# Optimization experiments

Hardware: AMD Instinct MI355X
Metric: run time of the kernel (lower is better)

## Reference

```python
import jax, jax.numpy as jnp
import numpy as np

B, N, E = 4, 10000, 160000
F_EXOG = 8
IN_DIM = 9          # 1 (pm25) + F_EXOG
HIST, PRED = 8, 12
HID = 64
GNN_OUT = 13
E_HID, E_OUT = 32, 30
GRU_IN = IN_DIM + GNN_OUT  # 22


def setup_inputs() -> dict:
    key = jax.random.key(0)
    ks = jax.random.split(key, 16)
    s = 0.1
    return {
        "pm25_hist": jax.random.normal(ks[0], (B, HIST, N, 1), jnp.float32),
        "feature": jax.random.normal(ks[1], (B, HIST + PRED, N, F_EXOG), jnp.float32),
        "edge_attr": jax.random.uniform(ks[2], (E, 2), jnp.float32),
        "wind_mean": jnp.array([2.0, 180.0], jnp.float32),
        "wind_std": jnp.array([1.5, 90.0], jnp.float32),
        # edge MLP: Linear(21->32), Sigmoid, Linear(32->30), Sigmoid
        "e_w1": jax.random.normal(ks[3], (2 * IN_DIM + 3, E_HID), jnp.float32) * s,
        "e_b1": jnp.zeros((E_HID,), jnp.float32),
        "e_w2": jax.random.normal(ks[4], (E_HID, E_OUT), jnp.float32) * s,
        "e_b2": jnp.zeros((E_OUT,), jnp.float32),
        # node MLP: Linear(30->13), Sigmoid
        "n_w": jax.random.normal(ks[5], (E_OUT, GNN_OUT), jnp.float32) * s,
        "n_b": jnp.zeros((GNN_OUT,), jnp.float32),
        # GRUCell(22 -> 64), torch layout: weight_ih (3H, in), weight_hh (3H, H)
        "gru_wi": jax.random.normal(ks[6], (3 * HID, GRU_IN), jnp.float32) * s,
        "gru_wh": jax.random.normal(ks[7], (3 * HID, HID), jnp.float32) * s,
        "gru_bi": jnp.zeros((3 * HID,), jnp.float32),
        "gru_bh": jnp.zeros((3 * HID,), jnp.float32),
        # fc_out: Linear(64 -> 1)
        "fc_w": jax.random.normal(ks[8], (HID, 1), jnp.float32) * s,
        "fc_b": jnp.zeros((1,), jnp.float32),
        "edge_index": jax.random.randint(ks[9], (2, E), 0, N, jnp.int64),
    }


def _forward(pm25_hist, feature, edge_attr, wind_mean, wind_std,
             e_w1, e_b1, e_w2, e_b2, n_w, n_b,
             gru_wi, gru_wh, gru_bi, gru_bh, fc_w, fc_b, edge_index):
    batch, _, n_nodes, _ = pm25_hist.shape
    src, tgt = edge_index[0], edge_index[1]

    # buffers precomputed in __init__ (torch.std uses ddof=1)
    edge_mean = edge_attr.mean(axis=0, keepdims=True)
    edge_std = jnp.maximum(jnp.std(edge_attr, axis=0, ddof=1, keepdims=True), 1e-6)
    edge_attr_norm = (edge_attr - edge_mean) / edge_std          # (E, 2)
    city_dist = jnp.maximum(edge_attr[:, 0], 1e-3)               # (E,)
    city_direc = edge_attr[:, 1]                                 # (E,)
    w_std = jnp.maximum(wind_std, 1e-6)

    def graph_gnn(x):                                            # x: (B, N, IN_DIM)
        node_src = x[:, src]                                     # (B, E, IN_DIM)
        node_tgt = x[:, tgt]
        wind = node_src[..., -2:] * w_std + wind_mean            # de-normalize
        speed = jnp.maximum(wind[..., 0], 0.0)                   # (B, E)
        wdir = jnp.deg2rad(wind[..., 1])
        theta = jnp.abs(city_direc - wdir)
        edge_w = jax.nn.relu(3.0 * speed * jnp.cos(theta) / city_dist)  # (B, E)
        ean = jnp.broadcast_to(edge_attr_norm, (x.shape[0], E, 2))
        h = jnp.concatenate([node_src, node_tgt, ean, edge_w[..., None]], axis=-1)
        h = jax.nn.sigmoid(h @ e_w1 + e_b1)
        h = jax.nn.sigmoid(h @ e_w2 + e_b2)                      # (B, E, E_OUT)
        agg = jnp.zeros((x.shape[0], n_nodes, E_OUT), x.dtype)
        agg = agg.at[:, tgt].add(h).at[:, src].add(-h)           # scatter add / sub
        return jax.nn.sigmoid(agg @ n_w + n_b)                   # (B, N, GNN_OUT)

    def gru_step(h, x):                                          # h,x: (B*N, .)
        gi = x @ gru_wi.T + gru_bi
        gh = h @ gru_wh.T + gru_bh
        i_r, i_z, i_n = jnp.split(gi, 3, axis=-1)
        h_r, h_z, h_n = jnp.split(gh, 3, axis=-1)
        r = jax.nn.sigmoid(i_r + h_r)
        z = jax.nn.sigmoid(i_z + h_z)
        n = jnp.tanh(i_n + r * h_n)
        return (1.0 - z) * n + z * h

    def step(carry, feat_t):
        hn, xn = carry                                           # (B*N,HID), (B,N,1)
        x = jnp.concatenate([xn, feat_t], axis=-1)               # (B, N, IN_DIM)
        x_gnn = graph_gnn(x)
        xc = jnp.concatenate([x_gnn, x], axis=-1).reshape(batch * n_nodes, -1)
        hn = gru_step(hn, xc)
        xn = hn.reshape(batch, n_nodes, HID) @ fc_w + fc_b       # (B, N, 1)
        return (hn, xn), xn[..., 0]

    hn0 = jnp.zeros((batch * n_nodes, HID), pm25_hist.dtype)
    xn0 = pm25_hist[:, -1]                                       # (B, N, 1)
    feats = jnp.swapaxes(feature[:, HIST:HIST + PRED], 0, 1)     # (PRED, B, N, F)
    _, preds = jax.lax.scan(step, (hn0, xn0), feats)             # (PRED, B, N)
    return jnp.transpose(preds, (1, 2, 0))                       # (B, N, PRED)


def reference(pm25_hist, feature, edge_attr, wind_mean, wind_std,
              e_w1, e_b1, e_w2, e_b2, n_w, n_b,
              gru_wi, gru_wh, gru_bi, gru_bh, fc_w, fc_b, edge_index):
    return _forward(pm25_hist, feature, edge_attr, wind_mean, wind_std,
                    e_w1, e_b1, e_w2, e_b2, n_w, n_b,
                    gru_wi, gru_wh, gru_bi, gru_bh, fc_w, fc_b, edge_index)
```

## Files before the change

### kernel.cpp

```cpp
#include <hip/hip_runtime.h>
#include <hip/hip_fp16.h>
#include <cstddef>

#define BB    4
#define NN    10000
#define EE    160000
#define BN    40000
#define HISTC 8
#define PREDC 12
#define TSTEP 20
#define FEX   8
#define HIDC  64
#define EHID  32
#define EOUTC 30
#define GOUTC 13
#define GINC  22

typedef float v2f __attribute__((ext_vector_type(2)));
typedef _Float16 v2h __attribute__((ext_vector_type(2)));

struct alignas(16) WPack {
    __half2 w[16];
    float   nw[14];
    float   b2;
    float   pad;
};

__device__ __forceinline__ float fast_rcp(float x) { return __builtin_amdgcn_rcpf(x); }
__device__ __forceinline__ float sigm(float x) {
    return fast_rcp(1.0f + __expf(-x));
}
__device__ __forceinline__ v2f sigm2(v2f x) {
    v2f r; r.x = sigm(x.x); r.y = sigm(x.y); return r;
}
__device__ __forceinline__ float tanh_fast(float x) {
    x = fminf(fmaxf(x, -15.0f), 15.0f);
    float e = __expf(2.0f * x);
    return (e - 1.0f) * fast_rcp(e + 1.0f);
}

__device__ __forceinline__ float dot2(__half2 a, __half2 b, float c) {
#if __has_builtin(__builtin_amdgcn_fdot2)
    union { __half2 h; v2h v; } ua, ub;
    ua.h = a; ub.h = b;
    return __builtin_amdgcn_fdot2(ua.v, ub.v, c, false);
#else
    float2 fa = __half22float2(a), fb = __half22float2(b);
    return c + fa.x * fb.x + fa.y * fb.y;
#endif
}

__global__ __launch_bounds__(256) void stats1_kernel(const float* __restrict__ ea,
                                                     double* __restrict__ part) {
    __shared__ double sm[256][4];
    int tid = threadIdx.x;
    double s0 = 0, s1 = 0, q0 = 0, q1 = 0;
    for (int e = blockIdx.x * 256 + tid; e < EE; e += 256 * 256) {
        float2 v = reinterpret_cast<const float2*>(ea)[e];
        double v0 = (double)v.x, v1 = (double)v.y;
        s0 += v0; q0 += v0 * v0;
        s1 += v1; q1 += v1 * v1;
    }
    sm[tid][0] = s0; sm[tid][1] = s1; sm[tid][2] = q0; sm[tid][3] = q1;
    __syncthreads();
    for (int off = 128; off > 0; off >>= 1) {
        if (tid < off)
            for (int k = 0; k < 4; k++) sm[tid][k] += sm[tid + off][k];
        __syncthreads();
    }
    if (tid == 0) {
        part[blockIdx.x * 4 + 0] = sm[0][0];
        part[blockIdx.x * 4 + 1] = sm[0][1];
        part[blockIdx.x * 4 + 2] = sm[0][2];
        part[blockIdx.x * 4 + 3] = sm[0][3];
    }
}

__global__ __launch_bounds__(256) void stats2_kernel(const double* __restrict__ part,
                                                     float* __restrict__ stats) {
    __shared__ double sm[256][4];
    int tid = threadIdx.x;
    sm[tid][0] = part[tid * 4 + 0];
    sm[tid][1] = part[tid * 4 + 1];
    sm[tid][2] = part[tid * 4 + 2];
    sm[tid][3] = part[tid * 4 + 3];
    __syncthreads();
    for (int off = 128; off > 0; off >>= 1) {
        if (tid < off)
            for (int k = 0; k < 4; k++) sm[tid][k] += sm[tid + off][k];
        __syncthreads();
    }
    if (tid == 0) {
        double m0 = sm[0][0] / EE, m1 = sm[0][1] / EE;
        double v0 = (sm[0][2] - sm[0][0] * sm[0][0] / EE) / (double)(EE - 1);
        double v1 = (sm[0][3] - sm[0][1] * sm[0][1] / EE) / (double)(EE - 1);
        float sd0 = fmaxf((float)sqrt(v0 > 0 ? v0 : 0.0), 1e-6f);
        float sd1 = fmaxf((float)sqrt(v1 > 0 ? v1 : 0.0), 1e-6f);
        stats[0] = (float)m0; stats[1] = (float)m1;
        stats[2] = 1.0f / sd0; stats[3] = 1.0f / sd1;
    }
}

__global__ __launch_bounds__(256) void edgepre_kernel(
    const float* __restrict__ ea, const float* __restrict__ stats,
    const int* __restrict__ eidx,
    int* __restrict__ deg_t, int* __restrict__ deg_s,
    float4* __restrict__ epre4)
{
    int e = blockIdx.x * 256 + threadIdx.x;
    if (e >= EE) return;
    float2 v = reinterpret_cast<const float2*>(ea)[e];
    float4 r;
    r.x = (v.x - stats[0]) * stats[2];
    r.y = (v.y - stats[1]) * stats[3];
    r.z = 1.0f / fmaxf(v.x, 1e-3f);
    r.w = v.y;
    epre4[e] = r;
    atomicAdd(&deg_s[eidx[e]], 1);
    atomicAdd(&deg_t[eidx[EE + e]], 1);
}

__global__ __launch_bounds__(256) void cvtw_kernel(
    const float* __restrict__ wi, const float* __restrict__ wh,
    const float* __restrict__ ew2, const float* __restrict__ eb2,
    const float* __restrict__ nw,
    __half* __restrict__ wi_h, __half* __restrict__ wh_h,
    WPack* __restrict__ wpack)
{
    int i = blockIdx.x * 256 + threadIdx.x;
    if (i < 192 * GINC) wi_h[i] = __float2half(wi[i]);
    if (i < 192 * HIDC) wh_h[i] = __float2half(wh[i]);
    if (i < EOUTC) {
        WPack wp;
        #pragma unroll
        for (int q = 0; q < 16; q++)
            wp.w[q] = __floats2half2_rn(ew2[(2 * q) * EOUTC + i],
                                        ew2[(2 * q + 1) * EOUTC + i]);
        #pragma unroll
        for (int j = 0; j < GOUTC; j++) wp.nw[j] = nw[i * GOUTC + j];
        wp.nw[13] = 0.f;
        wp.b2 = eb2[i];
        wp.pad = 0.f;
        wpack[i] = wp;
    }
}

__global__ void initxn_kernel(const float* __restrict__ pm, float* __restrict__ xn) {
    int i = blockIdx.x * 256 + threadIdx.x;
    if (i >= BN) return;
    int b = i / NN, n = i - b * NN;
    xn[i] = pm[(b * HISTC + (HISTC - 1)) * NN + n];
}

__global__ __launch_bounds__(1024) void scan_kernel(
    const int* __restrict__ deg_t, const int* __restrict__ deg_s,
    int* __restrict__ off_t, int* __restrict__ off_s,
    int* __restrict__ cnt_t, int* __restrict__ cnt_s)
{
    __shared__ int pt[1024], ps[1024];
    int tid = threadIdx.x;
    int base = tid * 10;
    int st = 0, ss = 0;
    for (int k = 0; k < 10; k++) {
        int i = base + k;
        if (i < NN) { st += deg_t[i]; ss += deg_s[i]; }
    }
    pt[tid] = st; ps[tid] = ss;
    __syncthreads();
    for (int off = 1; off < 1024; off <<= 1) {
        int vt = (tid >= off) ? pt[tid - off] : 0;
        int vs = (tid >= off) ? ps[tid - off] : 0;
        __syncthreads();
        pt[tid] += vt; ps[tid] += vs;
        __syncthreads();
    }
    int ext = (tid == 0) ? 0 : pt[tid - 1];
    int exs = (tid == 0) ? 0 : ps[tid - 1];
    for (int k = 0; k < 10; k++) {
        int i = base + k;
        if (i < NN) {
            off_t[i] = ext; cnt_t[i] = ext;
            off_s[i] = exs; cnt_s[i] = exs;
            ext += deg_t[i]; exs += deg_s[i];
        }
    }
    if (tid == 0) { off_t[NN] = EE; off_s[NN] = EE; }
}

__global__ void fillperm_kernel(const int* __restrict__ eidx,
                                const float4* __restrict__ epre4,
                                int* __restrict__ cnt_t, int* __restrict__ cnt_s,
                                int4* __restrict__ eT, float4* __restrict__ epreT)
{
    int e = blockIdx.x * 256 + threadIdx.x;
    if (e >= EE) return;
    int s = eidx[e];
    int g = eidx[EE + e];
    int pt = atomicAdd(&cnt_t[g], 1);
    int ps = atomicAdd(&cnt_s[s], 1);
    int4 r; r.x = s; r.y = g; r.z = ps; r.w = 0;
    eT[pt] = r;
    epreT[pt] = epre4[e];
}

__global__ __launch_bounds__(256) void pre_kernel(
    float* __restrict__ xncur, const float* __restrict__ feature, int t,
    const float* __restrict__ xp,
    const float* __restrict__ fb,
    const float* __restrict__ ew1,
    const float* __restrict__ wmean, const float* __restrict__ wstd,
    __half* __restrict__ preS, __half* __restrict__ preT,
    float2* __restrict__ wind2, float* __restrict__ out)
{
    __shared__ alignas(16) float w1s[18 * EHID];
    for (int i = threadIdx.x; i < 18 * EHID; i += 256) w1s[i] = ew1[i];
    __syncthreads();
    int idx = blockIdx.x * 256 + threadIdx.x;
    if (idx >= BN * 8) return;
    int i = idx >> 3;
    int c = idx & 7;
    int b = i / NN, n = i - b * NN;
    float x0;
    if (t == 0) {
        x0 = xncur[i];
    } else {
        x0 = (xp[i] + xp[BN + i]) + (xp[2 * BN + i] + xp[3 * BN + i]) + fb[0];
        if (c == 0) {
            xncur[i] = x0;
            out[(size_t)i * PREDC + (t - 1)] = x0;
        }
    }
    float x[9];
    x[0] = x0;
    {
        const float4* fp = reinterpret_cast<const float4*>(
            feature + (((size_t)b * TSTEP + HISTC + t) * NN + n) * FEX);
        float4 u = fp[0], v = fp[1];
        x[1] = u.x; x[2] = u.y; x[3] = u.z; x[4] = u.w;
        x[5] = v.x; x[6] = v.y; x[7] = v.z; x[8] = v.w;
    }
    float4 aS = {0.f, 0.f, 0.f, 0.f}, aT = {0.f, 0.f, 0.f, 0.f};
    #pragma unroll
    for (int k = 0; k < 9; k++) {
        float4 wS = reinterpret_cast<const float4*>(&w1s[k * EHID])[c];
        float4 wT = reinterpret_cast<const float4*>(&w1s[(9 + k) * EHID])[c];
        aS.x += x[k] * wS.x; aS.y += x[k] * wS.y; aS.z += x[k] * wS.z; aS.w += x[k] * wS.w;
        aT.x += x[k] * wT.x; aT.y += x[k] * wT.y; aT.z += x[k] * wT.z; aT.w += x[k] * wT.w;
    }
    union { uint2 u; __half h[4]; } sv, tv;
    sv.h[0] = __float2half(aS.x); sv.h[1] = __float2half(aS.y);
    sv.h[2] = __float2half(aS.z); sv.h[3] = __float2half(aS.w);
    tv.h[0] = __float2half(aT.x); tv.h[1] = __float2half(aT.y);
    tv.h[2] = __float2half(aT.z); tv.h[3] = __float2half(aT.w);
    reinterpret_cast<uint2*>(preS + (size_t)i * EHID)[c] = sv.u;
    reinterpret_cast<uint2*>(preT + (size_t)i * EHID)[c] = tv.u;
    if (c == 1) {
        float sd0 = fmaxf(wstd[0], 1e-6f), sd1 = fmaxf(wstd[1], 1e-6f);
        float speed = fmaxf(x[7] * sd0 + wmean[0], 0.f);
        float wdir  = (x[8] * sd1 + wmean[1]) * 0.017453292519943295f;
        float2 wv; wv.x = 3.0f * speed; wv.y = wdir;
        wind2[i] = wv;
    }
}

__global__ __launch_bounds__(256) void finalout_kernel(
    const float* __restrict__ xp, const float* __restrict__ fb,
    float* __restrict__ out)
{
    int i = blockIdx.x * 256 + threadIdx.x;
    if (i >= BN) return;
    out[(size_t)i * PREDC + (PREDC - 1)] =
        (xp[i] + xp[BN + i]) + (xp[2 * BN + i] + xp[3 * BN + i]) + fb[0];
}

__global__ __launch_bounds__(256) void edge_kernel(
    const int4* __restrict__ eT, const float4* __restrict__ epreT,
    const __half* __restrict__ preS, const __half* __restrict__ preT,
    const float2* __restrict__ wind2,
    const float* __restrict__ ew1, const float* __restrict__ eb1,
    const WPack* __restrict__ wpack,
    __half* __restrict__ h3t, __half* __restrict__ h3s)
{
    int i = blockIdx.x * 256 + threadIdx.x;
    int b = blockIdx.y;
    int4 et = eT[i];
    int s = et.x, g = et.y, ps = et.z;
    float4 ep = epreT[i];

    size_t iS = (size_t)b * NN + s, iT = (size_t)b * NN + g;
    float2 wv2 = wind2[iS];
    float ew = fmaxf(wv2.x * __cosf(fabsf(ep.w - wv2.y)) * ep.z, 0.f);

    union alignas(16) { uint4 u[4]; __half2 h2[16]; } RS, RT;
    {
        const uint4* p;
        p = reinterpret_cast<const uint4*>(preS + iS * EHID);
        RS.u[0] = p[0]; RS.u[1] = p[1]; RS.u[2] = p[2]; RS.u[3] = p[3];
        p = reinterpret_cast<const uint4*>(preT + iT * EHID);
        RT.u[0] = p[0]; RT.u[1] = p[1]; RT.u[2] = p[2]; RT.u[3] = p[3];
    }

    const v2f* W18 = reinterpret_cast<const v2f*>(ew1 + 18 * EHID);
    const v2f* W19 = reinterpret_cast<const v2f*>(ew1 + 19 * EHID);
    const v2f* W20 = reinterpret_cast<const v2f*>(ew1 + 20 * EHID);
    const v2f* B1  = reinterpret_cast<const v2f*>(eb1);
    float ean0 = ep.x, ean1 = ep.y;
    __half2 h1h[16];
    #pragma unroll
    for (int q = 0; q < 16; q++) {
        v2f u = W18[q] * ean0 + W19[q] * ean1 + B1[q] + W20[q] * ew;
        float2 rs = __half22float2(RS.h2[q]);
        float2 rt = __half22float2(RT.h2[q]);
        u.x += rs.x + rt.x;
        u.y += rs.y + rt.y;
        v2f sg = sigm2(u);
        h1h[q] = __floats2half2_rn(sg.x, sg.y);
    }

    v2f h3p[7];
    #pragma unroll
    for (int j = 0; j < 7; j++) { h3p[j].x = 0.f; h3p[j].y = 0.f; }
    for (int o = 0; o < EOUTC; o++) {
        const WPack* W = wpack + o;
        float acc0 = W->b2, acc1 = 0.f;
        #pragma unroll
        for (int q = 0; q < 16; q += 2) {
            acc0 = dot2(h1h[q],     W->w[q],     acc0);
            acc1 = dot2(h1h[q + 1], W->w[q + 1], acc1);
        }
        float h2v = sigm(acc0 + acc1);
        const v2f* nr = reinterpret_cast<const v2f*>(W->nw);
        #pragma unroll
        for (int j = 0; j < 7; j++) h3p[j] += nr[j] * h2v;
    }

    union alignas(16) { uint4 u[2]; __half2 h2[8]; } r;
    #pragma unroll
    for (int j = 0; j < 7; j++) r.h2[j] = __floats2half2_rn(h3p[j].x, h3p[j].y);
    r.h2[7] = __floats2half2_rn(0.f, 0.f);
    {
        __half* oT = h3t + ((size_t)b * EE + i) * 16;
        reinterpret_cast<uint4*>(oT)[0] = r.u[0];
        reinterpret_cast<uint4*>(oT)[1] = r.u[1];
        __half* oS = h3s + ((size_t)b * EE + ps) * 16;
        reinterpret_cast<uint4*>(oS)[0] = r.u[0];
        reinterpret_cast<uint4*>(oS)[1] = r.u[1];
    }
}

__global__ __launch_bounds__(256) void gather_kernel(
    const __half* __restrict__ h3t, const __half* __restrict__ h3s,
    const int* __restrict__ off_t, const int* __restrict__ off_s,
    const float* __restrict__ nb, const float* __restrict__ xncur,
    __half* __restrict__ xcagg)
{
    int n = (blockIdx.x * 256 + threadIdx.x) >> 6;
    if (n >= NN) return;
    n = __builtin_amdgcn_readfirstlane(n);
    int lane = threadIdx.x & 63;
    int b   = lane >> 4;
    int e4  = (lane >> 2) & 3;
    int chq = lane & 3;

    const __half* ht = h3t + (size_t)b * ((size_t)EE * 16) + chq * 4;
    const __half* hs = h3s + (size_t)b * ((size_t)EE * 16) + chq * 4;

    float a0 = 0.f, a1 = 0.f, a2 = 0.f, a3 = 0.f;
    {
        int i0 = off_t[n], i1 = off_t[n + 1];
        for (int i = i0 + e4; i < i1; i += 4) {
            uint2 v = *reinterpret_cast<const uint2*>(ht + (size_t)i * 16);
            float2 f01 = __half22float2(*reinterpret_cast<__half2*>(&v.x));
            float2 f23 = __half22float2(*reinterpret_cast<__half2*>(&v.y));
            a0 += f01.x; a1 += f01.y; a2 += f23.x; a3 += f23.y;
        }
    }
    {
        int i0 = off_s[n], i1 = off_s[n + 1];
        for (int i = i0 + e4; i < i1; i += 4) {
            uint2 v = *reinterpret_cast<const uint2*>(hs + (size_t)i * 16);
            float2 f01 = __half22float2(*reinterpret_cast<__half2*>(&v.x));
            float2 f23 = __half22float2(*reinterpret_cast<__half2*>(&v.y));
            a0 -= f01.x; a1 -= f01.y; a2 -= f23.x; a3 -= f23.y;
        }
    }
    a0 += __shfl_xor(a0, 4); a1 += __shfl_xor(a1, 4);
    a2 += __shfl_xor(a2, 4); a3 += __shfl_xor(a3, 4);
    a0 += __shfl_xor(a0, 8); a1 += __shfl_xor(a1, 8);
    a2 += __shfl_xor(a2, 8); a3 += __shfl_xor(a3, 8);

    if (e4 == 0) {
        int c0 = chq * 4;
        float nb0 = nb[c0 < GOUTC ? c0 : GOUTC - 1];
        float nb1 = nb[c0 + 1 < GOUTC ? c0 + 1 : GOUTC - 1];
        float nb2 = nb[c0 + 2 < GOUTC ? c0 + 2 : GOUTC - 1];
        float nb3 = nb[c0 + 3 < GOUTC ? c0 + 3 : GOUTC - 1];
        float v0 = (c0 + 0 < GOUTC) ? sigm(a0 + nb0) : 0.f;
        float v1 = (c0 + 1 < GOUTC) ? sigm(a1 + nb1)
                 : ((c0 + 1 == GOUTC) ? xncur[(size_t)b * NN + n] : 0.f);
        float v2 = (c0 + 2 < GOUTC) ? sigm(a2 + nb2) : 0.f;
        float v3 = (c0 + 3 < GOUTC) ? sigm(a3 + nb3) : 0.f;
        union { uint2 u; __half h[4]; } o;
        o.h[0] = __float2half(v0); o.h[1] = __float2half(v1);
        o.h[2] = __float2half(v2); o.h[3] = __float2half(v3);
        *reinterpret_cast<uint2*>(xcagg + ((size_t)b * NN + n) * 16 + c0) = o.u;
    }
}

__global__ __launch_bounds__(256) void node_kernel(
    const __half* __restrict__ xcagg, const float* __restrict__ feature, int t,
    const __half* __restrict__ wi_h, const __half* __restrict__ wh_h,
    const float* __restrict__ bi, const float* __restrict__ bh,
    const float* __restrict__ fw,
    const __half2* __restrict__ hnold, __half2* __restrict__ hnnew,
    float* __restrict__ xp)
{
    __shared__ float xpart[4][64];
    int lane = threadIdx.x & 63;
    int wav  = threadIdx.x >> 6;
    int jb   = blockIdx.y;
    int node = blockIdx.x * 64 + lane;
    int b = node / NN;
    int n = node - b * NN;

    __half2 xch[11];
    {
        union alignas(16) { uint4 u[2]; __half2 h2[8]; } X;
        const uint4* xp16 = reinterpret_cast<const uint4*>(xcagg + (size_t)node * 16);
        X.u[0] = xp16[0]; X.u[1] = xp16[1];
        #pragma unroll
        for (int p = 0; p < 7; p++) xch[p] = X.h2[p];
    }
    {
        const float4* fp = reinterpret_cast<const float4*>(
            feature + (((size_t)b * TSTEP + HISTC + t) * NN + n) * FEX);
        float4 u = fp[0], v = fp[1];
        xch[7]  = __floats2half2_rn(u.x, u.y);
        xch[8]  = __floats2half2_rn(u.z, u.w);
        xch[9]  = __floats2half2_rn(v.x, v.y);
        xch[10] = __floats2half2_rn(v.z, v.w);
    }

    __half2 hh[32];
    #pragma unroll
    for (int p = 0; p < 32; p++) hh[p] = hnold[(size_t)p * BN + node];

    float xsum = 0.f;
    #pragma unroll
    for (int jj2 = 0; jj2 < 2; jj2++) {
        int j0 = __builtin_amdgcn_readfirstlane(jb * 16 + wav * 4 + jj2 * 2);
        union { __half2 h; __half v[2]; } holdw;
        holdw.h = hnold[(size_t)(j0 >> 1) * BN + node];
        float hnew2[2];
        #pragma unroll
        for (int d = 0; d < 2; d++) {
            int j = j0 + d;
            float ir = bi[j], iz = bi[64 + j], in_ = bi[128 + j];
            const __half2* wr0 = reinterpret_cast<const __half2*>(wi_h + (size_t)j * GINC);
            const __half2* wr1 = reinterpret_cast<const __half2*>(wi_h + (size_t)(64 + j) * GINC);
            const __half2* wr2 = reinterpret_cast<const __half2*>(wi_h + (size_t)(128 + j) * GINC);
            #pragma unroll
            for (int p = 0; p < 11; p++) {
                ir  = dot2(xch[p], wr0[p], ir);
                iz  = dot2(xch[p], wr1[p], iz);
                in_ = dot2(xch[p], wr2[p], in_);
            }
            float hr0 = bh[j], hz0 = bh[64 + j], hn0 = bh[128 + j];
            float hr1 = 0.f, hz1 = 0.f, hn1 = 0.f;
            const __half2* vr0 = reinterpret_cast<const __half2*>(wh_h + (size_t)j * HIDC);
            const __half2* vr1 = reinterpret_cast<const __half2*>(wh_h + (size_t)(64 + j) * HIDC);
            const __half2* vr2 = reinterpret_cast<const __half2*>(wh_h + (size_t)(128 + j) * HIDC);
            #pragma unroll
            for (int p = 0; p < 32; p += 2) {
                hr0 = dot2(hh[p],     vr0[p],     hr0);
                hz0 = dot2(hh[p],     vr1[p],     hz0);
                hn0 = dot2(hh[p],     vr2[p],     hn0);
                hr1 = dot2(hh[p + 1], vr0[p + 1], hr1);
                hz1 = dot2(hh[p + 1], vr1[p + 1], hz1);
                hn1 = dot2(hh[p + 1], vr2[p + 1], hn1);
            }
            float r  = sigm(ir + hr0 + hr1);
            float z  = sigm(iz + hz0 + hz1);
            float nn = tanh_fast(in_ + r * (hn0 + hn1));
            float hold = __half2float(holdw.v[d]);
            float hnew = (1.f - z) * nn + z * hold;
            hnew2[d] = hnew;
            xsum += hnew * fw[j];
        }
        hnnew[(size_t)(j0 >> 1) * BN + node] = __floats2half2_rn(hnew2[0], hnew2[1]);
    }
    xpart[wav][lane] = xsum;
    __syncthreads();
    if (wav == 0) {
        float tot = xpart[0][lane] + xpart[1][lane] + xpart[2][lane] + xpart[3][lane];
        xp[(size_t)jb * BN + node] = tot;
    }
}

extern "C" void kernel_launch(void* const* d_in, const int* in_sizes, int n_in,
                              void* d_out, int out_size, void* d_ws, size_t ws_size,
                              hipStream_t stream)
{
    const float* pm    = (const float*)d_in[0];
    const float* feat  = (const float*)d_in[1];
    const float* ea    = (const float*)d_in[2];
    const float* wmean = (const float*)d_in[3];
    const float* wstd  = (const float*)d_in[4];
    const float* ew1   = (const float*)d_in[5];
    const float* eb1   = (const float*)d_in[6];
    const float* ew2   = (const float*)d_in[7];
    const float* eb2   = (const float*)d_in[8];
    const float* nw    = (const float*)d_in[9];
    const float* nb    = (const float*)d_in[10];
    const float* wi    = (const float*)d_in[11];
    const float* wh    = (const float*)d_in[12];
    const float* bi    = (const float*)d_in[13];
    const float* bh    = (const float*)d_in[14];
    const float* fw    = (const float*)d_in[15];
    const float* fb    = (const float*)d_in[16];
    const int*   eidx  = (const int*)d_in[17];
    float* out = (float*)d_out;

    char* w = (char*)d_ws;
    double* partd = (double*)w;                    w += 256 * 4 * sizeof(double);
    float*  stats = (float*)w;                     w += 16 * sizeof(float);
    WPack*  wpack = (WPack*)w;                     w += EOUTC * sizeof(WPack);
    float4* epre4 = (float4*)w;                    w += (size_t)EE * sizeof(float4);
    float4* epreT = (float4*)w;                    w += (size_t)EE * sizeof(float4);
    float*  xncur = (float*)w;                     w += (size_t)BN * sizeof(float);
    float*  xp    = (float*)w;                     w += (size_t)4 * BN * sizeof(float);
    __half2* hnA  = (__half2*)w;                   w += (size_t)32 * BN * sizeof(__half2);
    __half2* hnB  = (__half2*)w;                   w += (size_t)32 * BN * sizeof(__half2);
    __half* xcagg = (__half*)w;                    w += (size_t)BN * 16 * sizeof(__half);
    __half* preS  = (__half*)w;                    w += (size_t)BN * EHID * sizeof(__half);
    __half* preT  = (__half*)w;                    w += (size_t)BN * EHID * sizeof(__half);
    float2* wind2 = (float2*)w;                    w += (size_t)BN * sizeof(float2);
    __half* h3t   = (__half*)w;                    w += (size_t)BB * EE * 16 * sizeof(__half);
    __half* h3s   = (__half*)w;                    w += (size_t)BB * EE * 16 * sizeof(__half);
    __half* wi_h  = (__half*)w;                    w += (size_t)192 * GINC * sizeof(__half);
    __half* wh_h  = (__half*)w;                    w += (size_t)192 * HIDC * sizeof(__half);
    int*    deg_t = (int*)w;                       w += NN * sizeof(int);
    int*    deg_s = (int*)w;                       w += NN * sizeof(int);
    int*    off_t = (int*)w;                       w += (NN + 1) * sizeof(int);
    int*    off_s = (int*)w;                       w += (NN + 1) * sizeof(int);
    int*    cnt_t = (int*)w;                       w += NN * sizeof(int);
    int*    cnt_s = (int*)w;                       w += NN * sizeof(int);
    int4*   eT    = (int4*)w;                      w += (size_t)EE * sizeof(int4);

    stats1_kernel<<<256, 256, 0, stream>>>(ea, partd);
    stats2_kernel<<<1, 256, 0, stream>>>(partd, stats);
    hipMemsetAsync(deg_t, 0, 2 * NN * sizeof(int), stream);
    edgepre_kernel<<<(EE + 255) / 256, 256, 0, stream>>>(
        ea, stats, eidx, deg_t, deg_s, epre4);
    cvtw_kernel<<<(192 * HIDC + 255) / 256, 256, 0, stream>>>(
        wi, wh, ew2, eb2, nw, wi_h, wh_h, wpack);
    initxn_kernel<<<(BN + 255) / 256, 256, 0, stream>>>(pm, xncur);
    hipMemsetAsync(hnA, 0, (size_t)32 * BN * sizeof(__half2), stream);
    scan_kernel<<<1, 1024, 0, stream>>>(deg_t, deg_s, off_t, off_s, cnt_t, cnt_s);
    fillperm_kernel<<<(EE + 255) / 256, 256, 0, stream>>>(
        eidx, epre4, cnt_t, cnt_s, eT, epreT);

    for (int t = 0; t < PREDC; t++) {
        const __half2* hnold = (t & 1) ? hnB : hnA;
        __half2*       hnnew = (t & 1) ? hnA : hnB;
        pre_kernel<<<(BN * 8 + 255) / 256, 256, 0, stream>>>(
            xncur, feat, t, xp, fb, ew1, wmean, wstd, preS, preT, wind2, out);
        edge_kernel<<<dim3(EE / 256, BB), 256, 0, stream>>>(
            eT, epreT, preS, preT, wind2, ew1, eb1, wpack, h3t, h3s);
        gather_kernel<<<(NN * 64 + 255) / 256, 256, 0, stream>>>(
            h3t, h3s, off_t, off_s, nb, xncur, xcagg);
        node_kernel<<<dim3(BN / 64, 4), 256, 0, stream>>>(
            xcagg, feat, t, wi_h, wh_h, bi, bh, fw, hnold, hnnew, xp);
    }
    finalout_kernel<<<(BN + 255) / 256, 256, 0, stream>>>(xp, fb, out);
}
```

Baseline: 1.045 ms.

## Compute edge MLP second layer and node projection with MFMA matrix instructions

```diff
diff --git a/kernel.cpp b/kernel.cpp
--- a/kernel.cpp
+++ b/kernel.cpp
@@ -18,6 +18,8 @@
 
 typedef float v2f __attribute__((ext_vector_type(2)));
 typedef _Float16 v2h __attribute__((ext_vector_type(2)));
+typedef _Float16 v8h __attribute__((ext_vector_type(8)));
+typedef float f32x4 __attribute__((ext_vector_type(4)));
 
 struct alignas(16) WPack {
     __half2 w[16];
@@ -125,23 +127,19 @@
     const float* __restrict__ ew2, const float* __restrict__ eb2,
     const float* __restrict__ nw,
     __half* __restrict__ wi_h, __half* __restrict__ wh_h,
-    WPack* __restrict__ wpack)
+    __half* __restrict__ w2b, __half* __restrict__ nwb)
 {
     int i = blockIdx.x * 256 + threadIdx.x;
     if (i < 192 * GINC) wi_h[i] = __float2half(wi[i]);
     if (i < 192 * HIDC) wh_h[i] = __float2half(wh[i]);
-    if (i < EOUTC) {
-        WPack wp;
-        #pragma unroll
-        for (int q = 0; q < 16; q++)
-            wp.w[q] = __floats2half2_rn(ew2[(2 * q) * EOUTC + i],
-                                        ew2[(2 * q + 1) * EOUTC + i]);
-        #pragma unroll
-        for (int j = 0; j < GOUTC; j++) wp.nw[j] = nw[i * GOUTC + j];
-        wp.nw[13] = 0.f;
-        wp.b2 = eb2[i];
-        wp.pad = 0.f;
-        wpack[i] = wp;
+    if (i < 32 * 32) {
+        int o = i >> 5, k = i & 31;
+        w2b[i] = (o < EOUTC) ? __float2half(ew2[k * EOUTC + o]) : __half(0.0f);
+    }
+    if (i < 16 * 32) {
+        int j = i >> 5, o = i & 31;
+        nwb[i] = (j < GOUTC && o < EOUTC) ? __float2half(nw[o * GOUTC + j])
+                                          : __half(0.0f);
     }
 }
 
@@ -273,23 +271,43 @@
         (xp[i] + xp[BN + i]) + (xp[2 * BN + i] + xp[3 * BN + i]) + fb[0];
 }
 
+#define H1STR 40
+#define S2STR 36
 __global__ __launch_bounds__(256) void edge_kernel(
     const int4* __restrict__ eT, const float4* __restrict__ epreT,
     const __half* __restrict__ preS, const __half* __restrict__ preT,
     const float2* __restrict__ wind2,
     const float* __restrict__ ew1, const float* __restrict__ eb1,
-    const WPack* __restrict__ wpack,
+    const __half* __restrict__ w2b, const __half* __restrict__ nwb,
+    const float* __restrict__ eb2,
     __half* __restrict__ h3t, __half* __restrict__ h3s)
 {
-    int i = blockIdx.x * 256 + threadIdx.x;
+    __shared__ alignas(16) __half h1s[256 * H1STR];
+    __shared__ alignas(16) __half s2s[4][16 * S2STR];
+    __shared__ alignas(16) __half h3x[256 * 16];
+
+    int tid  = threadIdx.x;
+    int lane = tid & 63, wv = tid >> 6;
+    int l15  = lane & 15, lk = lane >> 4;
+    int i = blockIdx.x * 256 + tid;
     int b = blockIdx.y;
     int4 et = eT[i];
     int s = et.x, g = et.y, ps = et.z;
     float4 ep = epreT[i];
 
     size_t iS = (size_t)b * NN + s, iT = (size_t)b * NN + g;
-    float2 wv2 = wind2[iS];
-    float ew = fmaxf(wv2.x * __cosf(fabsf(ep.w - wv2.y)) * ep.z, 0.f);
+    float2 wvd = wind2[iS];
+    float ew = fmaxf(wvd.x * __cosf(fabsf(ep.w - wvd.y)) * ep.z, 0.f);
+
+    v8h bw2a, bw2b, bnw;
+    {
+        union { uint4 u; v8h h; } t;
+        t.u = *reinterpret_cast<const uint4*>(w2b + l15 * 32 + lk * 8);        bw2a = t.h;
+        t.u = *reinterpret_cast<const uint4*>(w2b + (16 + l15) * 32 + lk * 8); bw2b = t.h;
+        t.u = *reinterpret_cast<const uint4*>(nwb + l15 * 32 + lk * 8);        bnw  = t.h;
+    }
+    float b2v0 = eb2[l15];
+    float b2v1 = eb2[(16 + l15) < EOUTC ? (16 + l15) : (EOUTC - 1)];
 
     union alignas(16) { uint4 u[4]; __half2 h2[16]; } RS, RT;
     {
@@ -305,7 +323,7 @@
     const v2f* W20 = reinterpret_cast<const v2f*>(ew1 + 20 * EHID);
     const v2f* B1  = reinterpret_cast<const v2f*>(eb1);
     float ean0 = ep.x, ean1 = ep.y;
-    __half2 h1h[16];
+    union alignas(16) { uint4 u[4]; __half2 h2[16]; } H1;
     #pragma unroll
     for (int q = 0; q < 16; q++) {
         v2f u = W18[q] * ean0 + W19[q] * ean1 + B1[q] + W20[q] * ew;
@@ -314,37 +332,57 @@
         u.x += rs.x + rt.x;
         u.y += rs.y + rt.y;
         v2f sg = sigm2(u);
-        h1h[q] = __floats2half2_rn(sg.x, sg.y);
-    }
-
-    v2f h3p[7];
+        H1.h2[q] = __floats2half2_rn(sg.x, sg.y);
+    }
+    {
+        uint4* dst = reinterpret_cast<uint4*>(h1s + tid * H1STR);
+        dst[0] = H1.u[0]; dst[1] = H1.u[1]; dst[2] = H1.u[2]; dst[3] = H1.u[3];
+    }
+
+    f32x4 zero = {0.f, 0.f, 0.f, 0.f};
+    __half* s2w = s2s[wv];
     #pragma unroll
-    for (int j = 0; j < 7; j++) { h3p[j].x = 0.f; h3p[j].y = 0.f; }
-    for (int o = 0; o < EOUTC; o++) {
-        const WPack* W = wpack + o;
-        float acc0 = W->b2, acc1 = 0.f;
+    for (int mt = 0; mt < 4; ++mt) {
+        v8h af;
+        {
+            union { uint4 u; v8h h; } t;
+            t.u = *reinterpret_cast<const uint4*>(
+                h1s + (wv * 64 + mt * 16 + l15) * H1STR + lk * 8);
+            af = t.h;
+        }
+        f32x4 a0 = __builtin_amdgcn_mfma_f32_16x16x32_f16(af, bw2a, zero, 0, 0, 0);
+        f32x4 a1 = __builtin_amdgcn_mfma_f32_16x16x32_f16(af, bw2b, zero, 0, 0, 0);
         #pragma unroll
-        for (int q = 0; q < 16; q += 2) {
-            acc0 = dot2(h1h[q],     W->w[q],     acc0);
-            acc1 = dot2(h1h[q + 1], W->w[q + 1], acc1);
-        }
-        float h2v = sigm(acc0 + acc1);
-        const v2f* nr = reinterpret_cast<const v2f*>(W->nw);
+        for (int q = 0; q < 4; ++q) {
+            int rl = lk * 4 + q;
+            s2w[rl * S2STR + l15]      = __float2half(sigm(a0[q] + b2v0));
+            s2w[rl * S2STR + 16 + l15] = __float2half(sigm(a1[q] + b2v1));
+        }
+        v8h a2;
+        {
+            union { uint2 u[2]; v8h h; } t;
+            const __half* p2 = s2w + l15 * S2STR + lk * 8;
+            t.u[0] = *reinterpret_cast<const uint2*>(p2);
+            t.u[1] = *reinterpret_cast<const uint2*>(p2 + 4);
+            a2 = t.h;
+        }
+        f32x4 h3a = __builtin_amdgcn_mfma_f32_16x16x32_f16(a2, bnw, zero, 0, 0, 0);
         #pragma unroll
-        for (int j = 0; j < 7; j++) h3p[j] += nr[j] * h2v;
-    }
-
-    union alignas(16) { uint4 u[2]; __half2 h2[8]; } r;
-    #pragma unroll
-    for (int j = 0; j < 7; j++) r.h2[j] = __floats2half2_rn(h3p[j].x, h3p[j].y);
-    r.h2[7] = __floats2half2_rn(0.f, 0.f);
+        for (int q = 0; q < 4; ++q) {
+            h3x[(wv * 64 + mt * 16 + lk * 4 + q) * 16 + l15] = __float2half(h3a[q]);
+        }
+    }
+
+    union alignas(16) { uint4 u[2]; } R;
+    R.u[0] = *reinterpret_cast<const uint4*>(h3x + tid * 16);
+    R.u[1] = *reinterpret_cast<const uint4*>(h3x + tid * 16 + 8);
     {
         __half* oT = h3t + ((size_t)b * EE + i) * 16;
-        reinterpret_cast<uint4*>(oT)[0] = r.u[0];
-        reinterpret_cast<uint4*>(oT)[1] = r.u[1];
+        reinterpret_cast<uint4*>(oT)[0] = R.u[0];
+        reinterpret_cast<uint4*>(oT)[1] = R.u[1];
         __half* oS = h3s + ((size_t)b * EE + ps) * 16;
-        reinterpret_cast<uint4*>(oS)[0] = r.u[0];
-        reinterpret_cast<uint4*>(oS)[1] = r.u[1];
+        reinterpret_cast<uint4*>(oS)[0] = R.u[0];
+        reinterpret_cast<uint4*>(oS)[1] = R.u[1];
     }
 }
 
@@ -524,7 +562,6 @@
     char* w = (char*)d_ws;
     double* partd = (double*)w;                    w += 256 * 4 * sizeof(double);
     float*  stats = (float*)w;                     w += 16 * sizeof(float);
-    WPack*  wpack = (WPack*)w;                     w += EOUTC * sizeof(WPack);
     float4* epre4 = (float4*)w;                    w += (size_t)EE * sizeof(float4);
     float4* epreT = (float4*)w;                    w += (size_t)EE * sizeof(float4);
     float*  xncur = (float*)w;                     w += (size_t)BN * sizeof(float);
@@ -539,6 +576,8 @@
     __half* h3s   = (__half*)w;                    w += (size_t)BB * EE * 16 * sizeof(__half);
     __half* wi_h  = (__half*)w;                    w += (size_t)192 * GINC * sizeof(__half);
     __half* wh_h  = (__half*)w;                    w += (size_t)192 * HIDC * sizeof(__half);
+    __half* w2b   = (__half*)w;                    w += (size_t)32 * 32 * sizeof(__half);
+    __half* nwb   = (__half*)w;                    w += (size_t)16 * 32 * sizeof(__half);
     int*    deg_t = (int*)w;                       w += NN * sizeof(int);
     int*    deg_s = (int*)w;                       w += NN * sizeof(int);
     int*    off_t = (int*)w;                       w += (NN + 1) * sizeof(int);
@@ -553,7 +592,7 @@
     edgepre_kernel<<<(EE + 255) / 256, 256, 0, stream>>>(
         ea, stats, eidx, deg_t, deg_s, epre4);
     cvtw_kernel<<<(192 * HIDC + 255) / 256, 256, 0, stream>>>(
-        wi, wh, ew2, eb2, nw, wi_h, wh_h, wpack);
+        wi, wh, ew2, eb2, nw, wi_h, wh_h, w2b, nwb);
     initxn_kernel<<<(BN + 255) / 256, 256, 0, stream>>>(pm, xncur);
     hipMemsetAsync(hnA, 0, (size_t)32 * BN * sizeof(__half2), stream);
     scan_kernel<<<1, 1024, 0, stream>>>(deg_t, deg_s, off_t, off_s, cnt_t, cnt_s);
@@ -566,7 +605,7 @@
         pre_kernel<<<(BN * 8 + 255) / 256, 256, 0, stream>>>(
             xncur, feat, t, xp, fb, ew1, wmean, wstd, preS, preT, wind2, out);
         edge_kernel<<<dim3(EE / 256, BB), 256, 0, stream>>>(
-            eT, epreT, preS, preT, wind2, ew1, eb1, wpack, h3t, h3s);
+            eT, epreT, preS, preT, wind2, ew1, eb1, w2b, nwb, eb2, h3t, h3s);
         gather_kernel<<<(NN * 64 + 255) / 256, 256, 0, stream>>>(
             h3t, h3s, off_t, off_s, nb, xncur, xcagg);
         node_kernel<<<dim3(BN / 64, 4), 256, 0, stream>>>(
```

Measured after the change: 928.6 us. 1.13x faster.
